# Optimization experiments

Measured on AMD Instinct MI355X. Metric: run time of the kernel, lower is better.

## Reference

```python
import jax, jax.numpy as jnp
import numpy as np

N_NODES = 50000
N_EDGES = 800000
N_GRAPHS = 256
IN_DIM = 128
HID = 512            # hidden_layer_size
H2 = HID // 2        # 256, conv channels
H4 = HID // 4        # 128


def _linear_init(key, fan_in, fan_out):
    kw, kb = jax.random.split(key)
    bound = 1.0 / np.sqrt(fan_in)
    W = jax.random.uniform(kw, (fan_in, fan_out), minval=-bound, maxval=bound, dtype=jnp.float32)
    b = jax.random.uniform(kb, (fan_out,), minval=-bound, maxval=bound, dtype=jnp.float32)
    return W, b


def setup_inputs() -> dict:
    key = jax.random.key(0)
    ks = jax.random.split(key, 8)
    x = jax.random.normal(ks[0], (N_NODES, IN_DIM), dtype=jnp.float32)
    edge_index = jax.random.randint(ks[1], (2, N_EDGES), 0, N_NODES, dtype=jnp.int64)
    batch = jnp.sort(jax.random.randint(ks[2], (N_NODES,), 0, N_GRAPHS, dtype=jnp.int64))
    W1, b1 = _linear_init(ks[3], IN_DIM, HID)
    Wc1, bc1 = _linear_init(ks[4], HID, H2)
    Wc2, bc2 = _linear_init(ks[5], H2, H2)
    W2, b2 = _linear_init(ks[6], H2, H4)
    W3, b3 = _linear_init(ks[7], H4, 1)
    return {"x": x, "edge_index": edge_index, "batch": batch,
            "W1": W1, "b1": b1, "Wc1": Wc1, "bc1": bc1,
            "Wc2": Wc2, "bc2": bc2, "W2": W2, "b2": b2, "W3": W3, "b3": b3}


def _gcn_conv(h, W, b, src, dst, norm):
    # PyG GCNConv: out = scatter_add(norm * (h @ W)[src] -> dst) + b
    hw = h @ W                                   # [N, C_out]
    msg = norm[:, None] * hw[src]                # [E+N, C_out] gather
    agg = jax.ops.segment_sum(msg, dst, num_segments=N_NODES)  # scatter-add
    return agg + b


def reference(x, edge_index, batch, W1, b1, Wc1, bc1, Wc2, bc2, W2, b2, W3, b3):
    # --- symmetric GCN normalization with self-loops (shared by both convs) ---
    loop = jnp.arange(N_NODES, dtype=edge_index.dtype)
    src = jnp.concatenate([edge_index[0], loop])
    dst = jnp.concatenate([edge_index[1], loop])
    deg = jax.ops.segment_sum(jnp.ones_like(dst, dtype=jnp.float32), dst, num_segments=N_NODES)
    dinv = jax.lax.rsqrt(deg)                    # deg >= 1 thanks to self-loops
    norm = dinv[src] * dinv[dst]                 # [E+N]

    h = jax.nn.relu(x @ W1 + b1)                 # lin1
    h = jax.nn.relu(_gcn_conv(h, Wc1, bc1, src, dst, norm))   # conv1
    h = jax.nn.relu(_gcn_conv(h, Wc2, bc2, src, dst, norm))   # conv2

    # global_mean_pool over graph ids
    sums = jax.ops.segment_sum(h, batch, num_segments=N_GRAPHS)
    counts = jax.ops.segment_sum(jnp.ones((N_NODES,), jnp.float32), batch, num_segments=N_GRAPHS)
    g = sums / jnp.maximum(counts, 1.0)[:, None]

    # F.dropout is identity in deterministic/eval reference
    g = jax.nn.relu(g @ W2 + b2)                 # lin2
    return g @ W3 + b3                           # lin3 -> [N_GRAPHS, 1]
```

## Files before the change

kernel.cpp:

```cpp
#include <hip/hip_runtime.h>
#include <hip/hip_bf16.h>

#define NN 50000
#define NE 800000
#define NG 256
#define DIN 128
#define DH 512
#define DC 256
#define DL 128
#define NB 49

#define XBF_OFF   0UL
#define H1BF_OFF  12800000UL
#define HWBF_OFF  64000000UL
#define H2BF_OFF  89600000UL
#define H3BF_OFF  115200000UL
#define W1T_OFF   140800000UL
#define WC1T_OFF  140931072UL
#define WC2T_OFF  141193216UL
#define CNT_OFF   141324288UL
#define FILL_OFF  141524288UL
#define DINV_OFF  141724288UL
#define RP_OFF    141924288UL
#define BSUM_OFF  142124416UL
#define EW_OFF    142124800UL

using bf16x8 = __attribute__((ext_vector_type(8))) short;
using f32x4  = __attribute__((ext_vector_type(4))) float;

__device__ __forceinline__ short f2bf(float f) {
  unsigned u = __builtin_bit_cast(unsigned, f);
  unsigned r = u + 0x7fffu + ((u >> 16) & 1u);
  return (short)(r >> 16);
}
__device__ __forceinline__ float bf2f(unsigned short u) {
  return __builtin_bit_cast(float, (unsigned)u << 16);
}

__device__ __forceinline__ void gload_lds16(const void* g, void* l) {
  typedef const __attribute__((address_space(1))) unsigned gu32;
  typedef __attribute__((address_space(3))) unsigned lu32;
  __builtin_amdgcn_global_load_lds((gu32*)g, (lu32*)l, 16, 0, 0);
}

__global__ void count_in(const int* __restrict__ dst, int* __restrict__ cnt) {
  int e = blockIdx.x * blockDim.x + threadIdx.x;
  if (e < NE) atomicAdd(&cnt[dst[e]], 1);
}

__global__ __launch_bounds__(1024) void scan_p1(const int* __restrict__ cnt,
                                                int* __restrict__ rowptr,
                                                int* __restrict__ bsum,
                                                float* __restrict__ dinv) {
  __shared__ int wsum[16];
  const int idx = blockIdx.x * 1024 + threadIdx.x;
  const int lane = threadIdx.x & 63, wid = threadIdx.x >> 6;
  int v = (idx < NN) ? cnt[idx] : 0;
  int incl = v;
  #pragma unroll
  for (int s = 1; s < 64; s <<= 1) {
    int t = __shfl_up(incl, s, 64);
    if (lane >= s) incl += t;
  }
  if (lane == 63) wsum[wid] = incl;
  __syncthreads();
  if (wid == 0 && lane < 16) {
    int w = wsum[lane];
    int wincl = w;
    #pragma unroll
    for (int s = 1; s < 16; s <<= 1) {
      int t = __shfl_up(wincl, s, 64);
      if (lane >= s) wincl += t;
    }
    wsum[lane] = wincl - w;
    if (lane == 15) bsum[blockIdx.x] = wincl;
  }
  __syncthreads();
  if (idx < NN) {
    rowptr[idx] = wsum[wid] + incl - v;
    dinv[idx] = 1.0f / sqrtf((float)(v + 1));
  }
}

__global__ void scan_p2(int* __restrict__ bsum, int* __restrict__ rowptr) {
  const int lane = threadIdx.x;
  int v = (lane < NB) ? bsum[lane] : 0;
  int incl = v;
  #pragma unroll
  for (int s = 1; s < 64; s <<= 1) {
    int t = __shfl_up(incl, s, 64);
    if (lane >= s) incl += t;
  }
  if (lane < NB) bsum[lane] = incl - v;
  if (lane == 63) rowptr[NN] = incl;
}

__global__ __launch_bounds__(1024) void scan_p3(int* __restrict__ rowptr,
                                                const int* __restrict__ bsum) {
  const int idx = blockIdx.x * 1024 + threadIdx.x;
  if (idx < NN && blockIdx.x > 0) rowptr[idx] += bsum[blockIdx.x];
}

__global__ void fill_csr(const int* __restrict__ src, const int* __restrict__ dst,
                         const int* __restrict__ rowptr, int* __restrict__ fill,
                         const float* __restrict__ dinv, unsigned* __restrict__ ewp) {
  int e = blockIdx.x * blockDim.x + threadIdx.x;
  if (e < NE) {
    int d = dst[e];
    int s = src[e];
    int pos = rowptr[d] + atomicAdd(&fill[d], 1);
    float w = dinv[d] * dinv[s];
    ewp[pos] = (unsigned)s | ((unsigned)(unsigned short)f2bf(w) << 16);
  }
}

__global__ void prep(const float* __restrict__ x, short* __restrict__ xbf,
                     const float* __restrict__ W1, short* __restrict__ W1t,
                     const float* __restrict__ Wc1, short* __restrict__ Wc1t,
                     const float* __restrict__ Wc2, short* __restrict__ Wc2t) {
  int idx = blockIdx.x * 256 + threadIdx.x;
  if (idx < 800000) {
    const float4* p = (const float4*)x + (long)idx * 2;
    float4 a = p[0], b = p[1];
    bf16x8 o;
    o[0] = f2bf(a.x); o[1] = f2bf(a.y); o[2] = f2bf(a.z); o[3] = f2bf(a.w);
    o[4] = f2bf(b.x); o[5] = f2bf(b.y); o[6] = f2bf(b.z); o[7] = f2bf(b.w);
    *(bf16x8*)(xbf + (long)idx * 8) = o;
  } else if (idx < 865536) {
    int j = idx - 800000;
    int n = j >> 7, k = j & 127;
    W1t[j] = f2bf(W1[k * DH + n]);
  } else if (idx < 996608) {
    int j = idx - 865536;
    int n = j >> 9, k = j & 511;
    Wc1t[j] = f2bf(Wc1[k * DC + n]);
  } else if (idx < 1062144) {
    int j = idx - 996608;
    int n = j >> 8, k = j & 255;
    Wc2t[j] = f2bf(Wc2[k * DC + n]);
  }
}

template<int DO_RELU, int HAS_BIAS>
__global__ __launch_bounds__(256) void gemm_mfma4(
    const short* __restrict__ A,
    const short* __restrict__ Bt,
    const float* __restrict__ bias,
    short* __restrict__ Cout, int M, int K, int N)
{
  __shared__ __align__(16) short As[128][64];
  __shared__ __align__(16) short Bs[128][64];
  const int tid  = threadIdx.x;
  const int lane = tid & 63;
  const int wave = tid >> 6;
  const int wr   = wave >> 1;
  const int wc   = wave & 1;
  const int bm = blockIdx.y * 128;
  const int bn = blockIdx.x * 128;

  const int srow = lane >> 3;
  const int scol = (lane & 7) * 8;

  f32x4 acc[4][4];
  #pragma unroll
  for (int m = 0; m < 4; ++m)
    #pragma unroll
    for (int n = 0; n < 4; ++n)
      acc[m][n] = f32x4{0.f, 0.f, 0.f, 0.f};

  const int fr = lane & 15;
  const int kb = (lane >> 4) * 8;

  for (int k0 = 0; k0 < K; k0 += 64) {
    #pragma unroll
    for (int j = 0; j < 4; ++j) {
      const int r = wave * 32 + j * 8;
      gload_lds16(A  + (long)(bm + r + srow) * K + k0 + scol, &As[r][0]);
      gload_lds16(Bt + (long)(bn + r + srow) * K + k0 + scol, &Bs[r][0]);
    }
    __syncthreads();
    #pragma unroll
    for (int kk = 0; kk < 2; ++kk) {
      bf16x8 af[4], bfr[4];
      #pragma unroll
      for (int m = 0; m < 4; ++m)
        af[m] = *(const bf16x8*)&As[wr * 64 + m * 16 + fr][kk * 32 + kb];
      #pragma unroll
      for (int n = 0; n < 4; ++n)
        bfr[n] = *(const bf16x8*)&Bs[wc * 64 + n * 16 + fr][kk * 32 + kb];
      #pragma unroll
      for (int m = 0; m < 4; ++m)
        #pragma unroll
        for (int n = 0; n < 4; ++n)
          acc[m][n] = __builtin_amdgcn_mfma_f32_16x16x32_bf16(af[m], bfr[n], acc[m][n], 0, 0, 0);
    }
    __syncthreads();
  }

  const int cr4 = (lane >> 4) * 4;
  const int cc  = lane & 15;
  #pragma unroll
  for (int m = 0; m < 4; ++m) {
    #pragma unroll
    for (int r = 0; r < 4; ++r) {
      int gm = bm + wr * 64 + m * 16 + cr4 + r;
      if (gm >= M) continue;
      #pragma unroll
      for (int n = 0; n < 4; ++n) {
        int gn = bn + wc * 64 + n * 16 + cc;
        float v = acc[m][n][r];
        if (HAS_BIAS) v += bias[gn];
        if (DO_RELU) v = fmaxf(v, 0.f);
        Cout[(long)gm * N + gn] = f2bf(v);
      }
    }
  }
}

__global__ __launch_bounds__(256) void aggregate_v6(
    const unsigned short* __restrict__ hw, const unsigned* __restrict__ ewp,
    const int* __restrict__ rowptr, const float* __restrict__ dinv,
    const float* __restrict__ bias, unsigned short* __restrict__ out)
{
  const int wid  = threadIdx.x >> 6;
  const int lane = threadIdx.x & 63;
  const int i = blockIdx.x * 4 + wid;
  if (i >= NN) return;
  const int c0 = lane * 4;
  const float di = dinv[i];

  ushort4 sv = *(const ushort4*)(hw + (long)i * DC + c0);
  const float dii = di * di;
  float acc0 = dii * bf2f(sv.x);
  float acc1 = dii * bf2f(sv.y);
  float acc2 = dii * bf2f(sv.z);
  float acc3 = dii * bf2f(sv.w);

  const int s0 = rowptr[i], s1 = rowptr[i + 1];
  int e = s0;
  for (; e + 8 <= s1; e += 8) {
    unsigned pk[8]; ushort4 vv[8];
    #pragma unroll
    for (int j = 0; j < 8; ++j) pk[j] = __builtin_nontemporal_load(ewp + e + j);
    #pragma unroll
    for (int j = 0; j < 8; ++j)
      vv[j] = *(const ushort4*)(hw + (long)(pk[j] & 0xffffu) * DC + c0);
    #pragma unroll
    for (int j = 0; j < 8; ++j) {
      float w = bf2f((unsigned short)(pk[j] >> 16));
      acc0 += w * bf2f(vv[j].x);
      acc1 += w * bf2f(vv[j].y);
      acc2 += w * bf2f(vv[j].z);
      acc3 += w * bf2f(vv[j].w);
    }
  }
  for (; e + 4 <= s1; e += 4) {
    unsigned pk[4]; ushort4 vv[4];
    #pragma unroll
    for (int j = 0; j < 4; ++j) pk[j] = __builtin_nontemporal_load(ewp + e + j);
    #pragma unroll
    for (int j = 0; j < 4; ++j)
      vv[j] = *(const ushort4*)(hw + (long)(pk[j] & 0xffffu) * DC + c0);
    #pragma unroll
    for (int j = 0; j < 4; ++j) {
      float w = bf2f((unsigned short)(pk[j] >> 16));
      acc0 += w * bf2f(vv[j].x);
      acc1 += w * bf2f(vv[j].y);
      acc2 += w * bf2f(vv[j].z);
      acc3 += w * bf2f(vv[j].w);
    }
  }
  for (; e < s1; ++e) {
    unsigned pk = __builtin_nontemporal_load(ewp + e);
    float w = bf2f((unsigned short)(pk >> 16));
    ushort4 v = *(const ushort4*)(hw + (long)(pk & 0xffffu) * DC + c0);
    acc0 += w * bf2f(v.x);
    acc1 += w * bf2f(v.y);
    acc2 += w * bf2f(v.z);
    acc3 += w * bf2f(v.w);
  }
  const float4 bv = *(const float4*)(bias + c0);
  ushort4 o;
  o.x = (unsigned short)f2bf(fmaxf(acc0 + bv.x, 0.f));
  o.y = (unsigned short)f2bf(fmaxf(acc1 + bv.y, 0.f));
  o.z = (unsigned short)f2bf(fmaxf(acc2 + bv.z, 0.f));
  o.w = (unsigned short)f2bf(fmaxf(acc3 + bv.w, 0.f));
  *(ushort4*)(out + (long)i * DC + c0) = o;
}

__global__ __launch_bounds__(256) void pool_mlp_v3(
    const unsigned short* __restrict__ h, const int* __restrict__ batch,
    const float* __restrict__ W2, const float* __restrict__ b2,
    const float* __restrict__ W3, const float* __restrict__ b3,
    float* __restrict__ out)
{
  __shared__ float part[4][DC];
  __shared__ float gmean[DC];
  __shared__ float red[DL];
  const int g = blockIdx.x;
  const int t = threadIdx.x;
  const int wid = t >> 6;
  const int lane = t & 63;
  const int c0 = lane * 4;

  int lo = 0, hi = NN;
  while (lo < hi) { int mid = (lo + hi) >> 1; if (batch[mid] < g) lo = mid + 1; else hi = mid; }
  const int start = lo;
  hi = NN;
  while (lo < hi) { int mid = (lo + hi) >> 1; if (batch[mid] < g + 1) lo = mid + 1; else hi = mid; }
  const int end = lo;

  float4 a0 = {0.f, 0.f, 0.f, 0.f}, a1 = {0.f, 0.f, 0.f, 0.f};
  int i = start + wid;
  for (; i + 4 < end; i += 8) {
    ushort4 v0 = *(const ushort4*)(h + (long)i * DC + c0);
    ushort4 v1 = *(const ushort4*)(h + (long)(i + 4) * DC + c0);
    a0.x += bf2f(v0.x); a0.y += bf2f(v0.y); a0.z += bf2f(v0.z); a0.w += bf2f(v0.w);
    a1.x += bf2f(v1.x); a1.y += bf2f(v1.y); a1.z += bf2f(v1.z); a1.w += bf2f(v1.w);
  }
  if (i < end) {
    ushort4 v0 = *(const ushort4*)(h + (long)i * DC + c0);
    a0.x += bf2f(v0.x); a0.y += bf2f(v0.y); a0.z += bf2f(v0.z); a0.w += bf2f(v0.w);
  }
  a0.x += a1.x; a0.y += a1.y; a0.z += a1.z; a0.w += a1.w;
  *(float4*)&part[wid][c0] = a0;
  __syncthreads();
  if (wid == 0) {
    const float inv = 1.0f / fmaxf((float)(end - start), 1.f);
    float4 s0 = *(const float4*)&part[0][c0];
    float4 s1 = *(const float4*)&part[1][c0];
    float4 s2 = *(const float4*)&part[2][c0];
    float4 s3 = *(const float4*)&part[3][c0];
    float4 m;
    m.x = (s0.x + s1.x + s2.x + s3.x) * inv;
    m.y = (s0.y + s1.y + s2.y + s3.y) * inv;
    m.z = (s0.z + s1.z + s2.z + s3.z) * inv;
    m.w = (s0.w + s1.w + s2.w + s3.w) * inv;
    *(float4*)&gmean[c0] = m;
  }
  __syncthreads();
  if (t < DL) {
    float acc = b2[t];
    for (int k = 0; k < DC; ++k) acc = fmaf(gmean[k], W2[k * DL + t], acc);
    red[t] = fmaxf(acc, 0.f) * W3[t];
  }
  __syncthreads();
  for (int s2 = 64; s2 > 0; s2 >>= 1) {
    if (t < s2) red[t] += red[t + s2];
    __syncthreads();
  }
  if (t == 0) out[g] = red[0] + b3[0];
}

extern "C" void kernel_launch(void* const* d_in, const int* in_sizes, int n_in,
                              void* d_out, int out_size, void* d_ws, size_t ws_size,
                              hipStream_t stream) {
  const float* x    = (const float*)d_in[0];
  const int*   ei   = (const int*)d_in[1];
  const int*   bat  = (const int*)d_in[2];
  const float* W1   = (const float*)d_in[3];
  const float* b1   = (const float*)d_in[4];
  const float* Wc1  = (const float*)d_in[5];
  const float* bc1  = (const float*)d_in[6];
  const float* Wc2  = (const float*)d_in[7];
  const float* bc2  = (const float*)d_in[8];
  const float* W2   = (const float*)d_in[9];
  const float* b2   = (const float*)d_in[10];
  const float* W3   = (const float*)d_in[11];
  const float* b3   = (const float*)d_in[12];
  float* out = (float*)d_out;

  char* ws = (char*)d_ws;
  short* xbf    = (short*)(ws + XBF_OFF);
  short* h1bf   = (short*)(ws + H1BF_OFF);
  unsigned short* hwbf = (unsigned short*)(ws + HWBF_OFF);
  unsigned short* h2bf = (unsigned short*)(ws + H2BF_OFF);
  unsigned short* h3bf = (unsigned short*)(ws + H3BF_OFF);
  short* W1t    = (short*)(ws + W1T_OFF);
  short* Wc1t   = (short*)(ws + WC1T_OFF);
  short* Wc2t   = (short*)(ws + WC2T_OFF);
  int*   cnt    = (int*)  (ws + CNT_OFF);
  int*   fill   = (int*)  (ws + FILL_OFF);
  float* dinv   = (float*)(ws + DINV_OFF);
  int*   rowptr = (int*)  (ws + RP_OFF);
  int*   bsum   = (int*)  (ws + BSUM_OFF);
  unsigned* ewp = (unsigned*)(ws + EW_OFF);

  const int* srcE = ei;
  const int* dstE = ei + NE;

  hipMemsetAsync(cnt, 0, 2 * NN * sizeof(int), stream);

  count_in<<<(NE + 255) / 256, 256, 0, stream>>>(dstE, cnt);
  scan_p1<<<NB, 1024, 0, stream>>>(cnt, rowptr, bsum, dinv);
  scan_p2<<<1, 64, 0, stream>>>(bsum, rowptr);
  scan_p3<<<NB, 1024, 0, stream>>>(rowptr, bsum);
  fill_csr<<<(NE + 255) / 256, 256, 0, stream>>>(srcE, dstE, rowptr, fill, dinv, ewp);

  prep<<<(1062144 + 255) / 256, 256, 0, stream>>>(x, xbf, W1, W1t, Wc1, Wc1t, Wc2, Wc2t);

  {
    dim3 grid(DH / 128, (NN + 127) / 128);
    gemm_mfma4<1, 1><<<grid, 256, 0, stream>>>(xbf, W1t, b1, h1bf, NN, DIN, DH);
  }
  {
    dim3 grid(DC / 128, (NN + 127) / 128);
    gemm_mfma4<0, 0><<<grid, 256, 0, stream>>>(h1bf, Wc1t, nullptr, (short*)hwbf, NN, DH, DC);
  }
  aggregate_v6<<<(NN + 3) / 4, 256, 0, stream>>>(hwbf, ewp, rowptr, dinv, bc1, h2bf);
  {
    dim3 grid(DC / 128, (NN + 127) / 128);
    gemm_mfma4<0, 0><<<grid, 256, 0, stream>>>((const short*)h2bf, Wc2t, nullptr, (short*)hwbf, NN, DC, DC);
  }
  aggregate_v6<<<(NN + 3) / 4, 256, 0, stream>>>(hwbf, ewp, rowptr, dinv, bc2, h3bf);

  pool_mlp_v3<<<NG, 256, 0, stream>>>(h3bf, bat, W2, b2, W3, b3, out);
}
```

Measured before the change: 321.0 us.

## Slice conv features into 32-channel panels and degree-sort nodes for aggregation

The conv GEMMs now write their output in eight column slices of 32 channels each (slice-major layout). Aggregation runs one block per slice and group of 32 nodes, with 8 lanes per node, so each slice's gathered working set is smaller and more cache-friendly. Nodes are ordered by in-degree through a histogram and counting sort, so the nodes in a wave have similar edge counts and less divergence. In exchange this adds extra setup kernels, reads each edge list eight times (once per slice), and writes the output rows in scattered order.

```diff
diff --git a/kernel.cpp b/kernel.cpp
--- a/kernel.cpp
+++ b/kernel.cpp
@@ -9,6 +9,7 @@
 #define DC 256
 #define DL 128
 #define NB 49
+#define SLW 32
 
 #define XBF_OFF   0UL
 #define H1BF_OFF  12800000UL
@@ -20,10 +21,14 @@
 #define WC2T_OFF  141193216UL
 #define CNT_OFF   141324288UL
 #define FILL_OFF  141524288UL
-#define DINV_OFF  141724288UL
-#define RP_OFF    141924288UL
-#define BSUM_OFF  142124416UL
-#define EW_OFF    142124800UL
+#define DHIST_OFF 141724288UL
+#define DFILL_OFF 141724544UL
+#define DINV_OFF  141724800UL
+#define RP_OFF    141924800UL
+#define BSUM_OFF  142124816UL
+#define DBASE_OFF 142125072UL
+#define EW_OFF    142125344UL
+#define NORD_OFF  145325344UL
 
 using bf16x8 = __attribute__((ext_vector_type(8))) short;
 using f32x4  = __attribute__((ext_vector_type(4))) float;
@@ -51,10 +56,13 @@
 __global__ __launch_bounds__(1024) void scan_p1(const int* __restrict__ cnt,
                                                 int* __restrict__ rowptr,
                                                 int* __restrict__ bsum,
-                                                float* __restrict__ dinv) {
+                                                float* __restrict__ dinv,
+                                                int* __restrict__ dhist) {
   __shared__ int wsum[16];
+  __shared__ int lhist[64];
   const int idx = blockIdx.x * 1024 + threadIdx.x;
   const int lane = threadIdx.x & 63, wid = threadIdx.x >> 6;
+  if (threadIdx.x < 64) lhist[threadIdx.x] = 0;
   int v = (idx < NN) ? cnt[idx] : 0;
   int incl = v;
   #pragma unroll
@@ -79,7 +87,10 @@
   if (idx < NN) {
     rowptr[idx] = wsum[wid] + incl - v;
     dinv[idx] = 1.0f / sqrtf((float)(v + 1));
-  }
+    atomicAdd(&lhist[min(v, 63)], 1);
+  }
+  __syncthreads();
+  if (threadIdx.x < 64 && lhist[threadIdx.x]) atomicAdd(&dhist[threadIdx.x], lhist[threadIdx.x]);
 }
 
 __global__ void scan_p2(int* __restrict__ bsum, int* __restrict__ rowptr) {
@@ -93,6 +104,18 @@
   }
   if (lane < NB) bsum[lane] = incl - v;
   if (lane == 63) rowptr[NN] = incl;
+}
+
+__global__ void scan_deg(const int* __restrict__ dhist, int* __restrict__ dbase) {
+  const int lane = threadIdx.x;
+  int v = dhist[lane];
+  int incl = v;
+  #pragma unroll
+  for (int s = 1; s < 64; s <<= 1) {
+    int t = __shfl_up(incl, s, 64);
+    if (lane >= s) incl += t;
+  }
+  dbase[lane] = incl - v;
 }
 
 __global__ __launch_bounds__(1024) void scan_p3(int* __restrict__ rowptr,
@@ -111,6 +134,16 @@
     int pos = rowptr[d] + atomicAdd(&fill[d], 1);
     float w = dinv[d] * dinv[s];
     ewp[pos] = (unsigned)s | ((unsigned)(unsigned short)f2bf(w) << 16);
+  }
+}
+
+__global__ void node_sort(const int* __restrict__ cnt, const int* __restrict__ dbase,
+                          int* __restrict__ dfill, int* __restrict__ nodeord) {
+  int i = blockIdx.x * 256 + threadIdx.x;
+  if (i < NN) {
+    int b = min(cnt[i], 63);
+    int pos = dbase[b] + atomicAdd(&dfill[b], 1);
+    nodeord[pos] = i;
   }
 }
 
@@ -141,7 +174,7 @@
   }
 }
 
-template<int DO_RELU, int HAS_BIAS>
+template<int DO_RELU, int HAS_BIAS, int C_SLICED>
 __global__ __launch_bounds__(256) void gemm_mfma4(
     const short* __restrict__ A,
     const short* __restrict__ Bt,
@@ -211,81 +244,70 @@
         float v = acc[m][n][r];
         if (HAS_BIAS) v += bias[gn];
         if (DO_RELU) v = fmaxf(v, 0.f);
-        Cout[(long)gm * N + gn] = f2bf(v);
+        long cidx = C_SLICED ? ((long)(gn >> 5) * ((long)NN * SLW) + (long)gm * SLW + (gn & 31))
+                             : ((long)gm * N + gn);
+        Cout[cidx] = f2bf(v);
       }
     }
   }
 }
 
-__global__ __launch_bounds__(256) void aggregate_v6(
-    const unsigned short* __restrict__ hw, const unsigned* __restrict__ ewp,
+__global__ __launch_bounds__(256) void aggregate_v8(
+    const unsigned short* __restrict__ hw,
+    const unsigned* __restrict__ ewp,
     const int* __restrict__ rowptr, const float* __restrict__ dinv,
-    const float* __restrict__ bias, unsigned short* __restrict__ out)
+    const int* __restrict__ nodeord, const float* __restrict__ bias,
+    unsigned short* __restrict__ out)
 {
-  const int wid  = threadIdx.x >> 6;
-  const int lane = threadIdx.x & 63;
-  const int i = blockIdx.x * 4 + wid;
-  if (i >= NN) return;
-  const int c0 = lane * 4;
-  const float di = dinv[i];
-
-  ushort4 sv = *(const ushort4*)(hw + (long)i * DC + c0);
-  const float dii = di * di;
-  float acc0 = dii * bf2f(sv.x);
-  float acc1 = dii * bf2f(sv.y);
-  float acc2 = dii * bf2f(sv.z);
-  float acc3 = dii * bf2f(sv.w);
-
+  const int slice = blockIdx.x & 7;
+  const int j = (blockIdx.x >> 3) * 32 + (threadIdx.x >> 3);
+  const int li = threadIdx.x & 7;
+  if (j >= NN) return;
+  const int i = nodeord[j];
+  const unsigned short* hwS = hw + (long)slice * ((long)NN * SLW) + li * 4;
+
+  float a0 = 0.f, a1 = 0.f, a2 = 0.f, a3 = 0.f;
   const int s0 = rowptr[i], s1 = rowptr[i + 1];
   int e = s0;
-  for (; e + 8 <= s1; e += 8) {
-    unsigned pk[8]; ushort4 vv[8];
-    #pragma unroll
-    for (int j = 0; j < 8; ++j) pk[j] = __builtin_nontemporal_load(ewp + e + j);
-    #pragma unroll
-    for (int j = 0; j < 8; ++j)
-      vv[j] = *(const ushort4*)(hw + (long)(pk[j] & 0xffffu) * DC + c0);
-    #pragma unroll
-    for (int j = 0; j < 8; ++j) {
-      float w = bf2f((unsigned short)(pk[j] >> 16));
-      acc0 += w * bf2f(vv[j].x);
-      acc1 += w * bf2f(vv[j].y);
-      acc2 += w * bf2f(vv[j].z);
-      acc3 += w * bf2f(vv[j].w);
-    }
-  }
   for (; e + 4 <= s1; e += 4) {
-    unsigned pk[4]; ushort4 vv[4];
-    #pragma unroll
-    for (int j = 0; j < 4; ++j) pk[j] = __builtin_nontemporal_load(ewp + e + j);
-    #pragma unroll
-    for (int j = 0; j < 4; ++j)
-      vv[j] = *(const ushort4*)(hw + (long)(pk[j] & 0xffffu) * DC + c0);
-    #pragma unroll
-    for (int j = 0; j < 4; ++j) {
-      float w = bf2f((unsigned short)(pk[j] >> 16));
-      acc0 += w * bf2f(vv[j].x);
-      acc1 += w * bf2f(vv[j].y);
-      acc2 += w * bf2f(vv[j].z);
-      acc3 += w * bf2f(vv[j].w);
-    }
+    unsigned pk0 = __builtin_nontemporal_load(ewp + e);
+    unsigned pk1 = __builtin_nontemporal_load(ewp + e + 1);
+    unsigned pk2 = __builtin_nontemporal_load(ewp + e + 2);
+    unsigned pk3 = __builtin_nontemporal_load(ewp + e + 3);
+    ushort4 v0 = *(const ushort4*)(hwS + (pk0 & 0xffffu) * SLW);
+    ushort4 v1 = *(const ushort4*)(hwS + (pk1 & 0xffffu) * SLW);
+    ushort4 v2 = *(const ushort4*)(hwS + (pk2 & 0xffffu) * SLW);
+    ushort4 v3 = *(const ushort4*)(hwS + (pk3 & 0xffffu) * SLW);
+    float w0 = bf2f((unsigned short)(pk0 >> 16));
+    float w1 = bf2f((unsigned short)(pk1 >> 16));
+    float w2 = bf2f((unsigned short)(pk2 >> 16));
+    float w3 = bf2f((unsigned short)(pk3 >> 16));
+    a0 += w0 * bf2f(v0.x); a1 += w0 * bf2f(v0.y); a2 += w0 * bf2f(v0.z); a3 += w0 * bf2f(v0.w);
+    a0 += w1 * bf2f(v1.x); a1 += w1 * bf2f(v1.y); a2 += w1 * bf2f(v1.z); a3 += w1 * bf2f(v1.w);
+    a0 += w2 * bf2f(v2.x); a1 += w2 * bf2f(v2.y); a2 += w2 * bf2f(v2.z); a3 += w2 * bf2f(v2.w);
+    a0 += w3 * bf2f(v3.x); a1 += w3 * bf2f(v3.y); a2 += w3 * bf2f(v3.z); a3 += w3 * bf2f(v3.w);
   }
   for (; e < s1; ++e) {
     unsigned pk = __builtin_nontemporal_load(ewp + e);
     float w = bf2f((unsigned short)(pk >> 16));
-    ushort4 v = *(const ushort4*)(hw + (long)(pk & 0xffffu) * DC + c0);
-    acc0 += w * bf2f(v.x);
-    acc1 += w * bf2f(v.y);
-    acc2 += w * bf2f(v.z);
-    acc3 += w * bf2f(v.w);
-  }
-  const float4 bv = *(const float4*)(bias + c0);
+    ushort4 v = *(const ushort4*)(hwS + (pk & 0xffffu) * SLW);
+    a0 += w * bf2f(v.x); a1 += w * bf2f(v.y); a2 += w * bf2f(v.z); a3 += w * bf2f(v.w);
+  }
+  {
+    const float di = dinv[i];
+    const float w = di * di;
+    ushort4 sv = *(const ushort4*)(hwS + (unsigned)i * SLW);
+    a0 += w * bf2f(sv.x); a1 += w * bf2f(sv.y); a2 += w * bf2f(sv.z); a3 += w * bf2f(sv.w);
+  }
+  const int c = slice * SLW + li * 4;
+  const float4 bv = *(const float4*)(bias + c);
   ushort4 o;
-  o.x = (unsigned short)f2bf(fmaxf(acc0 + bv.x, 0.f));
-  o.y = (unsigned short)f2bf(fmaxf(acc1 + bv.y, 0.f));
-  o.z = (unsigned short)f2bf(fmaxf(acc2 + bv.z, 0.f));
-  o.w = (unsigned short)f2bf(fmaxf(acc3 + bv.w, 0.f));
-  *(ushort4*)(out + (long)i * DC + c0) = o;
+  o.x = (unsigned short)f2bf(fmaxf(a0 + bv.x, 0.f));
+  o.y = (unsigned short)f2bf(fmaxf(a1 + bv.y, 0.f));
+  o.z = (unsigned short)f2bf(fmaxf(a2 + bv.z, 0.f));
+  o.w = (unsigned short)f2bf(fmaxf(a3 + bv.w, 0.f));
+  unsigned long long pk = __builtin_bit_cast(unsigned long long, o);
+  __builtin_nontemporal_store(pk, (unsigned long long*)(out + (long)i * DC + c));
 }
 
 __global__ __launch_bounds__(256) void pool_mlp_v3(
@@ -381,38 +403,44 @@
   short* Wc2t   = (short*)(ws + WC2T_OFF);
   int*   cnt    = (int*)  (ws + CNT_OFF);
   int*   fill   = (int*)  (ws + FILL_OFF);
+  int*   dhist  = (int*)  (ws + DHIST_OFF);
+  int*   dfill  = (int*)  (ws + DFILL_OFF);
   float* dinv   = (float*)(ws + DINV_OFF);
   int*   rowptr = (int*)  (ws + RP_OFF);
   int*   bsum   = (int*)  (ws + BSUM_OFF);
+  int*   dbase  = (int*)  (ws + DBASE_OFF);
   unsigned* ewp = (unsigned*)(ws + EW_OFF);
+  int*   nodeord= (int*)  (ws + NORD_OFF);
 
   const int* srcE = ei;
   const int* dstE = ei + NE;
 
-  hipMemsetAsync(cnt, 0, 2 * NN * sizeof(int), stream);
+  hipMemsetAsync(cnt, 0, 2 * NN * sizeof(int) + 512, stream);
 
   count_in<<<(NE + 255) / 256, 256, 0, stream>>>(dstE, cnt);
-  scan_p1<<<NB, 1024, 0, stream>>>(cnt, rowptr, bsum, dinv);
+  scan_p1<<<NB, 1024, 0, stream>>>(cnt, rowptr, bsum, dinv, dhist);
   scan_p2<<<1, 64, 0, stream>>>(bsum, rowptr);
+  scan_deg<<<1, 64, 0, stream>>>(dhist, dbase);
   scan_p3<<<NB, 1024, 0, stream>>>(rowptr, bsum);
   fill_csr<<<(NE + 255) / 256, 256, 0, stream>>>(srcE, dstE, rowptr, fill, dinv, ewp);
+  node_sort<<<(NN + 255) / 256, 256, 0, stream>>>(cnt, dbase, dfill, nodeord);
 
   prep<<<(1062144 + 255) / 256, 256, 0, stream>>>(x, xbf, W1, W1t, Wc1, Wc1t, Wc2, Wc2t);
 
   {
     dim3 grid(DH / 128, (NN + 127) / 128);
-    gemm_mfma4<1, 1><<<grid, 256, 0, stream>>>(xbf, W1t, b1, h1bf, NN, DIN, DH);
+    gemm_mfma4<1, 1, 0><<<grid, 256, 0, stream>>>(xbf, W1t, b1, h1bf, NN, DIN, DH);
   }
   {
     dim3 grid(DC / 128, (NN + 127) / 128);
-    gemm_mfma4<0, 0><<<grid, 256, 0, stream>>>(h1bf, Wc1t, nullptr, (short*)hwbf, NN, DH, DC);
-  }
-  aggregate_v6<<<(NN + 3) / 4, 256, 0, stream>>>(hwbf, ewp, rowptr, dinv, bc1, h2bf);
+    gemm_mfma4<0, 0, 1><<<grid, 256, 0, stream>>>(h1bf, Wc1t, nullptr, (short*)hwbf, NN, DH, DC);
+  }
+  aggregate_v8<<<8 * ((NN + 31) / 32), 256, 0, stream>>>(hwbf, ewp, rowptr, dinv, nodeord, bc1, h2bf);
   {
     dim3 grid(DC / 128, (NN + 127) / 128);
-    gemm_mfma4<0, 0><<<grid, 256, 0, stream>>>((const short*)h2bf, Wc2t, nullptr, (short*)hwbf, NN, DC, DC);
-  }
-  aggregate_v6<<<(NN + 3) / 4, 256, 0, stream>>>(hwbf, ewp, rowptr, dinv, bc2, h3bf);
+    gemm_mfma4<0, 0, 1><<<grid, 256, 0, stream>>>((const short*)h2bf, Wc2t, nullptr, (short*)hwbf, NN, DC, DC);
+  }
+  aggregate_v8<<<8 * ((NN + 31) / 32), 256, 0, stream>>>(hwbf, ewp, rowptr, dinv, nodeord, bc2, h3bf);
 
   pool_mlp_v3<<<NG, 256, 0, stream>>>(h3bf, bat, W2, b2, W3, b3, out);
 }
```

After: 561.6 us. 1.75x slower.
